# Optimization experiments

Hardware: AMD Instinct MI355X
Metric: run time of the kernel (lower is better)

## Reference

```python
import jax, jax.numpy as jnp
import numpy as np

N_RES = 2_000_000
N_DOM = 2
B_WIN = 100
S_STRIDE = 10
HIDDEN = 128


def _build_windows():
    # Faithful port of the __init__ index construction.
    nb_per_res = B_WIN // S_STRIDE
    balance = B_WIN - S_STRIDE + 1
    start = np.maximum(np.arange(N_RES) + balance - B_WIN, 0)
    start = start // S_STRIDE + (start % S_STRIDE != 0).astype(np.int64)
    bs = start[:, None] + np.arange(nb_per_res)[None, :]
    return bs.astype(np.int32)


def setup_inputs() -> dict:
    key = jax.random.key(0)
    ks = jax.random.split(key, 7)
    bs_per_res = _build_windows()
    nb_windows = int(bs_per_res[-1, -1]) + 1  # 200009
    # weights near 1 (original inits to ones) so products stay well-scaled
    weights = jax.random.uniform(ks[0], (nb_windows, N_DOM), minval=0.5, maxval=1.5, dtype=jnp.float32)
    latent_variables = jax.random.normal(ks[1], (6,), dtype=jnp.float32)
    features = jax.random.normal(ks[2], (2, 50), dtype=jnp.float32)  # replaces torch.randn((2,50))
    W1 = jax.random.normal(ks[3], (53, HIDDEN), dtype=jnp.float32) * 0.1
    b1 = jnp.zeros((HIDDEN,), dtype=jnp.float32)
    W2 = jax.random.normal(ks[4], (HIDDEN, 3), dtype=jnp.float32) * 0.1
    b2 = jnp.zeros((3,), dtype=jnp.float32)
    local_frame = jax.random.normal(ks[5], (3, 3), dtype=jnp.float32)
    atom_absolute_positions = jax.random.normal(ks[6], (3 * N_RES, 3), dtype=jnp.float32)
    return {
        'weights': weights,
        'latent_variables': latent_variables,
        'features': features,
        'W1': W1, 'b1': b1, 'W2': W2, 'b2': b2,
        'local_frame': local_frame,
        'atom_absolute_positions': atom_absolute_positions,
        'bs_per_res': jnp.asarray(bs_per_res),
    }


def multiply_windows_weights(weights, bs_per_res):
    # gather: (N_res, nb_per_res, N_dom); product over the window axis, softmax over domains
    gathered = weights[bs_per_res]
    weights_per_residue = jnp.prod(gathered, axis=1)
    return jax.nn.softmax(weights_per_residue, axis=1)


def reference(weights, latent_variables, features, W1, b1, W2, b2,
              local_frame, atom_absolute_positions, bs_per_res):
    attn = multiply_windows_weights(weights, bs_per_res)  # (N_res, N_dom)
    # features_and_latent: (2, 53)
    fl = jnp.concatenate([features, latent_variables.reshape(2, 3)], axis=1)
    h = jax.nn.relu(fl @ W1 + b1)
    scalars_per_domain = h @ W2 + b2  # (N_dom, 3)
    # deform_structure: note module stores local_frame transposed
    translation_vectors = scalars_per_domain @ local_frame.T  # (N_dom, 3)
    translation_per_residue = attn @ translation_vectors      # (N_res, 3)
    new_atom_positions = atom_absolute_positions + jnp.repeat(translation_per_residue, 3, axis=0)
    return new_atom_positions, attn, translation_per_residue
```

## Files before the change

kernel.cpp:

```cpp
#include <hip/hip_runtime.h>

#define N_RES   2000000
#define HIDDEN  128

__global__ void mlp_kernel(const float* __restrict__ latent,
                           const float* __restrict__ features,
                           const float* __restrict__ W1,
                           const float* __restrict__ b1,
                           const float* __restrict__ W2,
                           const float* __restrict__ b2,
                           const float* __restrict__ lf,
                           float* __restrict__ tv_out)
{
    __shared__ float h[2][HIDDEN];
    __shared__ float s[2][3];
    const int tid = threadIdx.x;
    const int d = tid >> 7;
    const int j = tid & 127;

    float acc = b1[j];
    #pragma unroll 10
    for (int k = 0; k < 50; ++k)
        acc += features[d * 50 + k] * W1[k * HIDDEN + j];
    #pragma unroll
    for (int k = 0; k < 3; ++k)
        acc += latent[d * 3 + k] * W1[(50 + k) * HIDDEN + j];
    h[d][j] = fmaxf(acc, 0.0f);
    __syncthreads();

    if (tid < 6) {
        const int dd = tid / 3, c = tid % 3;
        float a = b2[c];
        #pragma unroll 16
        for (int k = 0; k < HIDDEN; ++k)
            a += h[dd][k] * W2[k * 3 + c];
        s[dd][c] = a;
    }
    __syncthreads();

    if (tid < 6) {
        const int dd = tid / 3, c = tid % 3;
        float a = 0.0f;
        #pragma unroll
        for (int k = 0; k < 3; ++k)
            a += s[dd][k] * lf[c * 3 + k];
        tv_out[dd * 3 + c] = a;
    }
}

__global__ __launch_bounds__(256)
void deform4_kernel(const float* __restrict__ weights,
                    const float* __restrict__ pos,
                    const float* __restrict__ tv,
                    float* __restrict__ out_pos,
                    float* __restrict__ out_attn,
                    float* __restrict__ out_trans)
{
    const int t = blockIdx.x * blockDim.x + threadIdx.x;
    if (t >= N_RES / 4) return;
    const int r0 = 4 * t;

    int st[4];
    #pragma unroll
    for (int i = 0; i < 4; ++i) {
        const int raw = max(r0 + i - 9, 0);
        st[i] = (raw + 9) / 10;
    }
    const int s0 = st[0];

    const float2* wb = (const float2*)weights + s0;
    float2 w[10];
    #pragma unroll
    for (int j = 0; j < 10; ++j) w[j] = wb[j];
    const float2 w10 = (st[3] > s0) ? wb[10] : make_float2(1.0f, 1.0f);

    float m0 = 1.0f, m1 = 1.0f;
    #pragma unroll
    for (int j = 1; j < 10; ++j) { m0 *= w[j].x; m1 *= w[j].y; }

    float tvx[6];
    #pragma unroll
    for (int k = 0; k < 6; ++k) tvx[k] = tv[k];

    float a[4][2];
    float tt[4][3];
    #pragma unroll
    for (int i = 0; i < 4; ++i) {
        const bool hi = st[i] > s0;
        const float p0 = hi ? m0 * w10.x : w[0].x * m0;
        const float p1 = hi ? m1 * w10.y : w[0].y * m1;
        const float mx  = fmaxf(p0, p1);
        const float e0  = __expf(p0 - mx);
        const float e1  = __expf(p1 - mx);
        const float inv = 1.0f / (e0 + e1);
        a[i][0] = e0 * inv;
        a[i][1] = e1 * inv;
        #pragma unroll
        for (int c = 0; c < 3; ++c)
            tt[i][c] = a[i][0] * tvx[c] + a[i][1] * tvx[3 + c];
    }

    float4* oat = (float4*)(out_attn + 8ll * t);
    oat[0] = make_float4(a[0][0], a[0][1], a[1][0], a[1][1]);
    oat[1] = make_float4(a[2][0], a[2][1], a[3][0], a[3][1]);

    float4* otr = (float4*)(out_trans + 12ll * t);
    otr[0] = make_float4(tt[0][0], tt[0][1], tt[0][2], tt[1][0]);
    otr[1] = make_float4(tt[1][1], tt[1][2], tt[2][0], tt[2][1]);
    otr[2] = make_float4(tt[2][2], tt[3][0], tt[3][1], tt[3][2]);

    const float4* pp = (const float4*)(pos + 36ll * t);
    float4*       op = (float4*)(out_pos + 36ll * t);
    #pragma unroll
    for (int k = 0; k < 9; ++k) {
        float4 v = pp[k];
        v.x += tt[(4 * k + 0) / 9][(4 * k + 0) % 3];
        v.y += tt[(4 * k + 1) / 9][(4 * k + 1) % 3];
        v.z += tt[(4 * k + 2) / 9][(4 * k + 2) % 3];
        v.w += tt[(4 * k + 3) / 9][(4 * k + 3) % 3];
        op[k] = v;
    }
}

extern "C" void kernel_launch(void* const* d_in, const int* in_sizes, int n_in,
                              void* d_out, int out_size, void* d_ws, size_t ws_size,
                              hipStream_t stream) {
    const float* weights  = (const float*)d_in[0];
    const float* latent   = (const float*)d_in[1];
    const float* features = (const float*)d_in[2];
    const float* W1       = (const float*)d_in[3];
    const float* b1       = (const float*)d_in[4];
    const float* W2       = (const float*)d_in[5];
    const float* b2       = (const float*)d_in[6];
    const float* lf       = (const float*)d_in[7];
    const float* pos      = (const float*)d_in[8];

    float* out = (float*)d_out;
    float* tv  = (float*)d_ws;

    mlp_kernel<<<1, 256, 0, stream>>>(latent, features, W1, b1, W2, b2, lf, tv);

    const int nthreads = N_RES / 4;
    const int blocks   = (nthreads + 255) / 256;
    deform4_kernel<<<blocks, 256, 0, stream>>>(
        weights, pos, tv,
        out,
        out + 18000000,
        out + 22000000);
}
```

Before: 246.2 us.

## Split deform into per-output block ranges with one float4 per thread

Replaces the per-4-residue thread, which read and wrote 36 floats of positions plus the attn and trans vectors, with a single grid whose block ranges each own one output array. Every thread now reads or writes exactly one float4, so the stores across a wavefront are fully contiguous. The cost is that each thread recomputes the window product and softmax for up to two residues, which means many redundant reads of the weights array (10-11 float2 loads per thread, mostly hitting cache) and extra ALU work. It also adds launch_bounds with min-blocks 4.

```diff
diff --git a/kernel.cpp b/kernel.cpp
--- a/kernel.cpp
+++ b/kernel.cpp
@@ -1,7 +1,13 @@
 #include <hip/hip_runtime.h>
 
-#define N_RES   2000000
-#define HIDDEN  128
+#define N_RES    2000000
+#define HIDDEN   128
+#define N_POS4   4500000
+#define N_ATTN4  1000000
+#define N_TRANS4 1500000
+#define B_POS    17579
+#define B_ATTN   3907
+#define B_TRANS  5860
 
 __global__ void mlp_kernel(const float* __restrict__ latent,
                            const float* __restrict__ features,
@@ -48,77 +54,130 @@
     }
 }
 
-__global__ __launch_bounds__(256)
-void deform4_kernel(const float* __restrict__ weights,
-                    const float* __restrict__ pos,
-                    const float* __restrict__ tv,
-                    float* __restrict__ out_pos,
-                    float* __restrict__ out_attn,
-                    float* __restrict__ out_trans)
-{
-    const int t = blockIdx.x * blockDim.x + threadIdx.x;
-    if (t >= N_RES / 4) return;
-    const int r0 = 4 * t;
-
-    int st[4];
-    #pragma unroll
-    for (int i = 0; i < 4; ++i) {
-        const int raw = max(r0 + i - 9, 0);
-        st[i] = (raw + 9) / 10;
-    }
-    const int s0 = st[0];
-
-    const float2* wb = (const float2*)weights + s0;
-    float2 w[10];
+__device__ __forceinline__ void load_windows(const float* __restrict__ weights,
+                                             int rLo, int rHi,
+                                             float2 w[10], float2& w10,
+                                             int& sLo, int& sHi)
+{
+    sLo = (max(rLo - 9, 0) + 9) / 10;
+    sHi = (max(rHi - 9, 0) + 9) / 10;
+    const float2* wb = (const float2*)weights + sLo;
     #pragma unroll
     for (int j = 0; j < 10; ++j) w[j] = wb[j];
-    const float2 w10 = (st[3] > s0) ? wb[10] : make_float2(1.0f, 1.0f);
-
+    w10 = (sLo <= 199998) ? wb[10] : make_float2(1.0f, 1.0f);
+}
+
+__device__ __forceinline__ void window_products(const float2 w[10], float2 w10,
+                                                int sLo, int sHi,
+                                                float& p0lo, float& p1lo,
+                                                float& p0hi, float& p1hi)
+{
     float m0 = 1.0f, m1 = 1.0f;
     #pragma unroll
     for (int j = 1; j < 10; ++j) { m0 *= w[j].x; m1 *= w[j].y; }
+    p0lo = w[0].x * m0;
+    p1lo = w[0].y * m1;
+    const bool shift = sHi > sLo;
+    p0hi = shift ? m0 * w10.x : p0lo;
+    p1hi = shift ? m1 * w10.y : p1lo;
+}
+
+__device__ __forceinline__ void softmax_t(float p0, float p1,
+                                          const float tvx[6],
+                                          float a[2], float t[3])
+{
+    const float mx  = fmaxf(p0, p1);
+    const float e0  = __expf(p0 - mx);
+    const float e1  = __expf(p1 - mx);
+    const float inv = 1.0f / (e0 + e1);
+    a[0] = e0 * inv;
+    a[1] = e1 * inv;
+    t[0] = a[0] * tvx[0] + a[1] * tvx[3];
+    t[1] = a[0] * tvx[1] + a[1] * tvx[4];
+    t[2] = a[0] * tvx[2] + a[1] * tvx[5];
+}
+
+__global__ __launch_bounds__(256, 4)
+void deform_kernel(const float* __restrict__ weights,
+                   const float* __restrict__ tv,
+                   const float* __restrict__ pos,
+                   float* __restrict__ out_pos,
+                   float* __restrict__ out_attn,
+                   float* __restrict__ out_trans)
+{
+    const int tid = threadIdx.x;
+    const int b   = blockIdx.x;
 
     float tvx[6];
     #pragma unroll
     for (int k = 0; k < 6; ++k) tvx[k] = tv[k];
 
-    float a[4][2];
-    float tt[4][3];
-    #pragma unroll
-    for (int i = 0; i < 4; ++i) {
-        const bool hi = st[i] > s0;
-        const float p0 = hi ? m0 * w10.x : w[0].x * m0;
-        const float p1 = hi ? m1 * w10.y : w[0].y * m1;
-        const float mx  = fmaxf(p0, p1);
-        const float e0  = __expf(p0 - mx);
-        const float e1  = __expf(p1 - mx);
-        const float inv = 1.0f / (e0 + e1);
-        a[i][0] = e0 * inv;
-        a[i][1] = e1 * inv;
+    if (b < B_POS) {
+        const int g = b * 256 + tid;
+        if (g >= N_POS4) return;
+        const int e0  = 4 * g;
+        const int rLo = e0 / 9;
+        const int rHi = (e0 + 3) / 9;
+
+        float2 w[10], w10; int sLo, sHi;
+        load_windows(weights, rLo, rHi, w, w10, sLo, sHi);
+        const float4 p = ((const float4*)pos)[g];
+
+        float p0lo, p1lo, p0hi, p1hi;
+        window_products(w, w10, sLo, sHi, p0lo, p1lo, p0hi, p1hi);
+        float aL[2], tL[3], aH[2], tH[3];
+        softmax_t(p0lo, p1lo, tvx, aL, tL);
+        softmax_t(p0hi, p1hi, tvx, aH, tH);
+
+        const float pin[4] = {p.x, p.y, p.z, p.w};
+        float o[4];
         #pragma unroll
-        for (int c = 0; c < 3; ++c)
-            tt[i][c] = a[i][0] * tvx[c] + a[i][1] * tvx[3 + c];
-    }
-
-    float4* oat = (float4*)(out_attn + 8ll * t);
-    oat[0] = make_float4(a[0][0], a[0][1], a[1][0], a[1][1]);
-    oat[1] = make_float4(a[2][0], a[2][1], a[3][0], a[3][1]);
-
-    float4* otr = (float4*)(out_trans + 12ll * t);
-    otr[0] = make_float4(tt[0][0], tt[0][1], tt[0][2], tt[1][0]);
-    otr[1] = make_float4(tt[1][1], tt[1][2], tt[2][0], tt[2][1]);
-    otr[2] = make_float4(tt[2][2], tt[3][0], tt[3][1], tt[3][2]);
-
-    const float4* pp = (const float4*)(pos + 36ll * t);
-    float4*       op = (float4*)(out_pos + 36ll * t);
-    #pragma unroll
-    for (int k = 0; k < 9; ++k) {
-        float4 v = pp[k];
-        v.x += tt[(4 * k + 0) / 9][(4 * k + 0) % 3];
-        v.y += tt[(4 * k + 1) / 9][(4 * k + 1) % 3];
-        v.z += tt[(4 * k + 2) / 9][(4 * k + 2) % 3];
-        v.w += tt[(4 * k + 3) / 9][(4 * k + 3) % 3];
-        op[k] = v;
+        for (int i = 0; i < 4; ++i) {
+            const int e = e0 + i;
+            const int c = e % 3;
+            const bool hi = (e / 9) > rLo;
+            o[i] = pin[i] + (hi ? tH[c] : tL[c]);
+        }
+        ((float4*)out_pos)[g] = make_float4(o[0], o[1], o[2], o[3]);
+    } else if (b < B_POS + B_ATTN) {
+        const int q = (b - B_POS) * 256 + tid;
+        if (q >= N_ATTN4) return;
+        const int rLo = 2 * q;
+        const int rHi = 2 * q + 1;
+
+        float2 w[10], w10; int sLo, sHi;
+        load_windows(weights, rLo, rHi, w, w10, sLo, sHi);
+        float p0lo, p1lo, p0hi, p1hi;
+        window_products(w, w10, sLo, sHi, p0lo, p1lo, p0hi, p1hi);
+        float aL[2], tL[3], aH[2], tH[3];
+        softmax_t(p0lo, p1lo, tvx, aL, tL);
+        softmax_t(p0hi, p1hi, tvx, aH, tH);
+
+        ((float4*)out_attn)[q] = make_float4(aL[0], aL[1], aH[0], aH[1]);
+    } else {
+        const int q = (b - B_POS - B_ATTN) * 256 + tid;
+        if (q >= N_TRANS4) return;
+        const int e0  = 4 * q;
+        const int rLo = e0 / 3;
+        const int rHi = (e0 + 3) / 3;
+
+        float2 w[10], w10; int sLo, sHi;
+        load_windows(weights, rLo, rHi, w, w10, sLo, sHi);
+        float p0lo, p1lo, p0hi, p1hi;
+        window_products(w, w10, sLo, sHi, p0lo, p1lo, p0hi, p1hi);
+        float aL[2], tL[3], aH[2], tH[3];
+        softmax_t(p0lo, p1lo, tvx, aL, tL);
+        softmax_t(p0hi, p1hi, tvx, aH, tH);
+
+        float o[4];
+        #pragma unroll
+        for (int i = 0; i < 4; ++i) {
+            const int e = e0 + i;
+            const int c = e % 3;
+            const bool hi = (e / 3) > rLo;
+            o[i] = hi ? tH[c] : tL[c];
+        }
+        ((float4*)out_trans)[q] = make_float4(o[0], o[1], o[2], o[3]);
     }
 }
 
@@ -140,10 +199,9 @@
 
     mlp_kernel<<<1, 256, 0, stream>>>(latent, features, W1, b1, W2, b2, lf, tv);
 
-    const int nthreads = N_RES / 4;
-    const int blocks   = (nthreads + 255) / 256;
-    deform4_kernel<<<blocks, 256, 0, stream>>>(
-        weights, pos, tv,
+    const int blocks = B_POS + B_ATTN + B_TRANS;
+    deform_kernel<<<blocks, 256, 0, stream>>>(
+        weights, tv, pos,
         out,
         out + 18000000,
         out + 22000000);
```

New measurement: 263.0 us. 6.8% more time.
